# Optimization experiments

Hardware: AMD Instinct MI355X
Metric: run time of the kernel (lower is better)

Reference implementation:

```python
import jax, jax.numpy as jnp
import numpy as np

ROUTING_ITERS = 3


def squash(s):
    # s: [..., O]; magnitude squashed into (0, 1)
    sq_norm = jnp.sum(s * s, axis=-1, keepdims=True)
    return (sq_norm / (1.0 + sq_norm)) * s / jnp.sqrt(sq_norm)


def setup_inputs() -> dict:
    key = jax.random.key(0)
    k1, k2 = jax.random.split(key)
    B, P, CI, N, CO = 512, 1152, 8, 10, 16
    x = jax.random.normal(k1, (B, P, CI), dtype=jnp.float32)
    W = jax.random.normal(k2, (N, P, CI, CO), dtype=jnp.float32)
    return {"x": x, "W": W}


def reference(x, W):
    # x: [B, P, CI], W: [N, P, CI, CO]
    # torch: u_hat = (x[None,:,:,None,:] @ W[:,None]) -> [N, B, P, 1, CO];
    # we drop the singleton dim: u_hat [N, B, P, CO]
    u_hat = jnp.einsum('bpi,npio->nbpo', x, W)
    b_ij = jnp.zeros_like(u_hat)
    v_j = None
    for it in range(ROUTING_ITERS):
        # softmax over previous-layer nodes P (torch dim=2 of [N,B,P,1,CO])
        c_ij = jax.nn.softmax(b_ij, axis=2)
        s_j = jnp.sum(c_ij * u_hat, axis=2, keepdims=True)  # [N, B, 1, CO]
        v_j = squash(s_j)
        if it < ROUTING_ITERS - 1:
            a_ij = jnp.sum(u_hat * v_j, axis=-1, keepdims=True)  # [N, B, P, 1]
            b_ij = b_ij + a_ij
    return v_j  # [N, B, 1, CO]
```

## Files before the change

kernel.cpp:

```cpp
#include <hip/hip_runtime.h>
#include <cstddef>

#define NN 10
#define NB 512
#define NP 1152
#define CI 8
#define CO 16
#define BLOCK 256
#define BT 2
#define PT 18

__device__ __forceinline__ float wred_sum_pg(float v) {
#pragma unroll
  for (int m = 4; m <= 32; m <<= 1) v += __shfl_xor(v, m);
  return v;
}
__device__ __forceinline__ float wred_max_pg(float v) {
#pragma unroll
  for (int m = 4; m <= 32; m <<= 1) v = fmaxf(v, __shfl_xor(v, m));
  return v;
}

__global__ __launch_bounds__(BLOCK, 2)
void caps_kernel(const float* __restrict__ x, const float* __restrict__ W,
                 float* __restrict__ out) {
  const int tid  = threadIdx.x;
  const int lane = tid & 63;
  const int wid  = tid >> 6;
  const int o4   = (tid & 3) << 2;
  const int pg   = tid >> 2;

  const int bid = blockIdx.x;
  const int n   = bid >> 8;
  const int b0  = (bid & 255) * BT;

  __shared__ float sred[BT][4][CO];
  __shared__ float mred[BT][4];
  __shared__ float zred[BT][4];
  __shared__ float vbuf[BT][CO];

  float4 u[BT][PT];
  float  bl[BT][PT];

  const float* Wn  = W + (size_t)n * NP * CI * CO + o4;
  const float* xb0 = x + (size_t)b0 * NP * CI;

#pragma unroll
  for (int k = 0; k < PT; ++k) {
    const int p = pg + 64 * k;
    const float* wrow = Wn + p * (CI * CO);
    const float* xr   = xb0 + p * CI;
    float xv0[CI], xv1[CI];
    *(float4*)&xv0[0] = *(const float4*)(xr);
    *(float4*)&xv0[4] = *(const float4*)(xr + 4);
    *(float4*)&xv1[0] = *(const float4*)(xr + NP * CI);
    *(float4*)&xv1[4] = *(const float4*)(xr + NP * CI + 4);
    float4 a0 = make_float4(0.f, 0.f, 0.f, 0.f);
    float4 a1 = make_float4(0.f, 0.f, 0.f, 0.f);
#pragma unroll
    for (int i = 0; i < CI; ++i) {
      const float4 wv = *(const float4*)(wrow + i * CO);
      a0.x = fmaf(xv0[i], wv.x, a0.x);
      a0.y = fmaf(xv0[i], wv.y, a0.y);
      a0.z = fmaf(xv0[i], wv.z, a0.z);
      a0.w = fmaf(xv0[i], wv.w, a0.w);
      a1.x = fmaf(xv1[i], wv.x, a1.x);
      a1.y = fmaf(xv1[i], wv.y, a1.y);
      a1.z = fmaf(xv1[i], wv.z, a1.z);
      a1.w = fmaf(xv1[i], wv.w, a1.w);
    }
    u[0][k] = a0; u[1][k] = a1;
    bl[0][k] = 0.f; bl[1][k] = 0.f;
  }

  float4 vv[BT];
  float  mm[BT], rz[BT];

#pragma unroll 1
  for (int it = 0; it < 3; ++it) {
    if (it > 0) {
#pragma unroll
      for (int bt = 0; bt < BT; ++bt) {
#pragma unroll
        for (int k = 0; k < PT; ++k) {
          float d = u[bt][k].x * vv[bt].x + u[bt][k].y * vv[bt].y
                  + u[bt][k].z * vv[bt].z + u[bt][k].w * vv[bt].w;
          d += __shfl_xor(d, 1);
          d += __shfl_xor(d, 2);
          bl[bt][k] += d;
        }
      }
#pragma unroll
      for (int bt = 0; bt < BT; ++bt) {
        float m = bl[bt][0];
#pragma unroll
        for (int k = 1; k < PT; ++k) m = fmaxf(m, bl[bt][k]);
        m = wred_max_pg(m);
        if (lane == 0) mred[bt][wid] = m;
      }
      __syncthreads();
#pragma unroll
      for (int bt = 0; bt < BT; ++bt)
        mm[bt] = fmaxf(fmaxf(mred[bt][0], mred[bt][1]),
                       fmaxf(mred[bt][2], mred[bt][3]));
#pragma unroll
      for (int bt = 0; bt < BT; ++bt) {
        float z = 0.f;
#pragma unroll
        for (int k = 0; k < PT; ++k) z += __expf(bl[bt][k] - mm[bt]);
        z = wred_sum_pg(z);
        if (lane == 0) zred[bt][wid] = z;
      }
      __syncthreads();
#pragma unroll
      for (int bt = 0; bt < BT; ++bt) {
        const float SZ = zred[bt][0] + zred[bt][1] + zred[bt][2] + zred[bt][3];
        rz[bt] = 1.f / SZ;
      }
    }

#pragma unroll
    for (int bt = 0; bt < BT; ++bt) {
      float4 ps = make_float4(0.f, 0.f, 0.f, 0.f);
      if (it == 0) {
#pragma unroll
        for (int k = 0; k < PT; ++k) {
          ps.x += u[bt][k].x; ps.y += u[bt][k].y;
          ps.z += u[bt][k].z; ps.w += u[bt][k].w;
        }
        const float c = 1.f / (float)NP;
        ps.x *= c; ps.y *= c; ps.z *= c; ps.w *= c;
      } else {
#pragma unroll
        for (int k = 0; k < PT; ++k) {
          const float e = __expf(bl[bt][k] - mm[bt]);
          ps.x = fmaf(e, u[bt][k].x, ps.x);
          ps.y = fmaf(e, u[bt][k].y, ps.y);
          ps.z = fmaf(e, u[bt][k].z, ps.z);
          ps.w = fmaf(e, u[bt][k].w, ps.w);
        }
        ps.x *= rz[bt]; ps.y *= rz[bt]; ps.z *= rz[bt]; ps.w *= rz[bt];
      }
#pragma unroll
      for (int m = 4; m <= 32; m <<= 1) {
        ps.x += __shfl_xor(ps.x, m);
        ps.y += __shfl_xor(ps.y, m);
        ps.z += __shfl_xor(ps.z, m);
        ps.w += __shfl_xor(ps.w, m);
      }
      if (lane < 4) *(float4*)&sred[bt][wid][lane << 2] = ps;
    }
    __syncthreads();

    if (tid < 32) {
      const int bt = tid >> 4, o = tid & 15;
      float s = sred[bt][0][o] + sred[bt][1][o] + sred[bt][2][o] + sred[bt][3][o];
      float sq = s * s;
#pragma unroll
      for (int m = 1; m <= 8; m <<= 1) sq += __shfl_xor(sq, m);
      const float nrm = sqrtf(sq);
      const float vj  = s * (nrm / (1.f + sq));
      if (it == 2) out[((size_t)n * NB + b0 + bt) * CO + o] = vj;
      else         vbuf[bt][o] = vj;
    }
    if (it < 2) {
      __syncthreads();
#pragma unroll
      for (int bt = 0; bt < BT; ++bt) vv[bt] = *(const float4*)&vbuf[bt][o4];
    }
  }
}

extern "C" void kernel_launch(void* const* d_in, const int* in_sizes, int n_in,
                              void* d_out, int out_size, void* d_ws, size_t ws_size,
                              hipStream_t stream) {
  const float* x = (const float*)d_in[0];
  const float* W = (const float*)d_in[1];
  float* out     = (float*)d_out;
  (void)in_sizes; (void)n_in; (void)out_size; (void)d_ws; (void)ws_size;
  const int grid = NN * (NB / BT);
  caps_kernel<<<grid, BLOCK, 0, stream>>>(x, W, out);
}
```

Before: 329.5 us.

## Stage x tile in LDS and loop over output capsules per block

Each block now loads x for 4 batch rows into swizzled shared memory once and loops over 5 output capsules, reusing that x tile for every capsule and reusing each W load across 4 batch rows. Block size doubles to 512 threads, and the softmax max/sum and weighted-sum reductions are fused so there is one fewer barrier per iteration. The aim is to cut redundant global traffic on x and W. The cost is about 147KB of dynamic LDS per block, which limits occupancy, and a grid of only 256 blocks with serial per-capsule work.

```diff
diff --git a/kernel.cpp b/kernel.cpp
--- a/kernel.cpp
+++ b/kernel.cpp
@@ -6,168 +6,175 @@
 #define NP 1152
 #define CI 8
 #define CO 16
-#define BLOCK 256
-#define BT 2
-#define PT 18
+#define BLOCK 512
+#define BT 4
+#define NPER 5
+#define PSLOTS 128
+#define PT 9
+#define NWAVE 8
 
-__device__ __forceinline__ float wred_sum_pg(float v) {
-#pragma unroll
-  for (int m = 4; m <= 32; m <<= 1) v += __shfl_xor(v, m);
-  return v;
-}
-__device__ __forceinline__ float wred_max_pg(float v) {
-#pragma unroll
-  for (int m = 4; m <= 32; m <<= 1) v = fmaxf(v, __shfl_xor(v, m));
-  return v;
-}
+#define X_FLOATS (BT * NP * CI)
+#define SRED_OFF (X_FLOATS)
+#define ZRED_OFF (SRED_OFF + NWAVE * BT * CO)
+#define MZ_OFF   (ZRED_OFF + NWAVE * BT)
+#define VBUF_OFF (MZ_OFF + NWAVE * BT)
+#define SMEM_FLOATS (VBUF_OFF + BT * CO)
+#define SMEM_BYTES (SMEM_FLOATS * 4)
 
-__global__ __launch_bounds__(BLOCK, 2)
+__global__
+__attribute__((amdgpu_flat_work_group_size(BLOCK, BLOCK), amdgpu_waves_per_eu(2, 2)))
 void caps_kernel(const float* __restrict__ x, const float* __restrict__ W,
                  float* __restrict__ out) {
+  extern __shared__ float smem[];
+  float4* X4 = (float4*)smem;
+
   const int tid  = threadIdx.x;
   const int lane = tid & 63;
   const int wid  = tid >> 6;
   const int o4   = (tid & 3) << 2;
-  const int pg   = tid >> 2;
+  const int ps   = tid >> 2;
 
   const int bid = blockIdx.x;
-  const int n   = bid >> 8;
-  const int b0  = (bid & 255) * BT;
+  const int nh  = bid & 1;
+  const int b0  = (bid >> 1) * BT;
 
-  __shared__ float sred[BT][4][CO];
-  __shared__ float mred[BT][4];
-  __shared__ float zred[BT][4];
-  __shared__ float vbuf[BT][CO];
+  {
+    const float4* xg = (const float4*)(x + (size_t)b0 * NP * CI);
+#pragma unroll
+    for (int k = 0; k < 18; ++k) {
+      const int j = tid + BLOCK * k;
+      X4[j ^ ((j >> 3) & 1)] = xg[j];
+    }
+  }
+  __syncthreads();
 
-  float4 u[BT][PT];
-  float  bl[BT][PT];
+  for (int ni = 0; ni < NPER; ++ni) {
+    const int n = nh * NPER + ni;
+    const float* Wn = W + ((size_t)n * NP + ps) * (CI * CO) + o4;
 
-  const float* Wn  = W + (size_t)n * NP * CI * CO + o4;
-  const float* xb0 = x + (size_t)b0 * NP * CI;
+    float4 u[BT][PT];
+    float  bl[BT][PT];
 
 #pragma unroll
-  for (int k = 0; k < PT; ++k) {
-    const int p = pg + 64 * k;
-    const float* wrow = Wn + p * (CI * CO);
-    const float* xr   = xb0 + p * CI;
-    float xv0[CI], xv1[CI];
-    *(float4*)&xv0[0] = *(const float4*)(xr);
-    *(float4*)&xv0[4] = *(const float4*)(xr + 4);
-    *(float4*)&xv1[0] = *(const float4*)(xr + NP * CI);
-    *(float4*)&xv1[4] = *(const float4*)(xr + NP * CI + 4);
-    float4 a0 = make_float4(0.f, 0.f, 0.f, 0.f);
-    float4 a1 = make_float4(0.f, 0.f, 0.f, 0.f);
+    for (int k = 0; k < PT; ++k) {
+      const int p = ps + PSLOTS * k;
+      const float* wrow = Wn + (size_t)k * (PSLOTS * CI * CO);
+      float4 wv[CI];
 #pragma unroll
-    for (int i = 0; i < CI; ++i) {
-      const float4 wv = *(const float4*)(wrow + i * CO);
-      a0.x = fmaf(xv0[i], wv.x, a0.x);
-      a0.y = fmaf(xv0[i], wv.y, a0.y);
-      a0.z = fmaf(xv0[i], wv.z, a0.z);
-      a0.w = fmaf(xv0[i], wv.w, a0.w);
-      a1.x = fmaf(xv1[i], wv.x, a1.x);
-      a1.y = fmaf(xv1[i], wv.y, a1.y);
-      a1.z = fmaf(xv1[i], wv.z, a1.z);
-      a1.w = fmaf(xv1[i], wv.w, a1.w);
-    }
-    u[0][k] = a0; u[1][k] = a1;
-    bl[0][k] = 0.f; bl[1][k] = 0.f;
-  }
-
-  float4 vv[BT];
-  float  mm[BT], rz[BT];
-
-#pragma unroll 1
-  for (int it = 0; it < 3; ++it) {
-    if (it > 0) {
+      for (int i = 0; i < CI; ++i) wv[i] = *(const float4*)(wrow + i * CO);
+      const int sw = (p >> 2) & 1;
 #pragma unroll
-      for (int bt = 0; bt < BT; ++bt) {
+      for (int b = 0; b < BT; ++b) {
+        const int c0 = (b * NP + p) << 1;
+        float xi[CI];
+        *(float4*)&xi[0] = X4[c0 ^ sw];
+        *(float4*)&xi[4] = X4[(c0 | 1) ^ sw];
+        float4 a = make_float4(0.f, 0.f, 0.f, 0.f);
 #pragma unroll
-        for (int k = 0; k < PT; ++k) {
-          float d = u[bt][k].x * vv[bt].x + u[bt][k].y * vv[bt].y
-                  + u[bt][k].z * vv[bt].z + u[bt][k].w * vv[bt].w;
-          d += __shfl_xor(d, 1);
-          d += __shfl_xor(d, 2);
-          bl[bt][k] += d;
+        for (int i = 0; i < CI; ++i) {
+          a.x = fmaf(xi[i], wv[i].x, a.x);
+          a.y = fmaf(xi[i], wv[i].y, a.y);
+          a.z = fmaf(xi[i], wv[i].z, a.z);
+          a.w = fmaf(xi[i], wv[i].w, a.w);
         }
-      }
-#pragma unroll
-      for (int bt = 0; bt < BT; ++bt) {
-        float m = bl[bt][0];
-#pragma unroll
-        for (int k = 1; k < PT; ++k) m = fmaxf(m, bl[bt][k]);
-        m = wred_max_pg(m);
-        if (lane == 0) mred[bt][wid] = m;
-      }
-      __syncthreads();
-#pragma unroll
-      for (int bt = 0; bt < BT; ++bt)
-        mm[bt] = fmaxf(fmaxf(mred[bt][0], mred[bt][1]),
-                       fmaxf(mred[bt][2], mred[bt][3]));
-#pragma unroll
-      for (int bt = 0; bt < BT; ++bt) {
-        float z = 0.f;
-#pragma unroll
-        for (int k = 0; k < PT; ++k) z += __expf(bl[bt][k] - mm[bt]);
-        z = wred_sum_pg(z);
-        if (lane == 0) zred[bt][wid] = z;
-      }
-      __syncthreads();
-#pragma unroll
-      for (int bt = 0; bt < BT; ++bt) {
-        const float SZ = zred[bt][0] + zred[bt][1] + zred[bt][2] + zred[bt][3];
-        rz[bt] = 1.f / SZ;
+        u[b][k] = a;
+        bl[b][k] = 0.f;
       }
     }
 
+    float4 vvb[BT];
+    float  mm[BT];
+
+#pragma unroll 1
+    for (int it = 0; it < 3; ++it) {
+      if (it > 0) {
 #pragma unroll
-    for (int bt = 0; bt < BT; ++bt) {
-      float4 ps = make_float4(0.f, 0.f, 0.f, 0.f);
-      if (it == 0) {
+        for (int b = 0; b < BT; ++b) {
+          float m = -1e30f;
 #pragma unroll
-        for (int k = 0; k < PT; ++k) {
-          ps.x += u[bt][k].x; ps.y += u[bt][k].y;
-          ps.z += u[bt][k].z; ps.w += u[bt][k].w;
+          for (int k = 0; k < PT; ++k) {
+            float d = u[b][k].x * vvb[b].x + u[b][k].y * vvb[b].y
+                    + u[b][k].z * vvb[b].z + u[b][k].w * vvb[b].w;
+            d += __shfl_xor(d, 1);
+            d += __shfl_xor(d, 2);
+            const float nb2 = bl[b][k] + d;
+            bl[b][k] = nb2;
+            m = fmaxf(m, nb2);
+          }
+#pragma unroll
+          for (int s = 4; s <= 32; s <<= 1) m = fmaxf(m, __shfl_xor(m, s));
+          if (lane == 0) smem[MZ_OFF + wid * BT + b] = m;
         }
-        const float c = 1.f / (float)NP;
-        ps.x *= c; ps.y *= c; ps.z *= c; ps.w *= c;
-      } else {
+        __syncthreads();
 #pragma unroll
-        for (int k = 0; k < PT; ++k) {
-          const float e = __expf(bl[bt][k] - mm[bt]);
-          ps.x = fmaf(e, u[bt][k].x, ps.x);
-          ps.y = fmaf(e, u[bt][k].y, ps.y);
-          ps.z = fmaf(e, u[bt][k].z, ps.z);
-          ps.w = fmaf(e, u[bt][k].w, ps.w);
+        for (int b = 0; b < BT; ++b) {
+          float m = smem[MZ_OFF + b];
+#pragma unroll
+          for (int w = 1; w < NWAVE; ++w) m = fmaxf(m, smem[MZ_OFF + w * BT + b]);
+          mm[b] = m;
         }
-        ps.x *= rz[bt]; ps.y *= rz[bt]; ps.z *= rz[bt]; ps.w *= rz[bt];
       }
+
 #pragma unroll
-      for (int m = 4; m <= 32; m <<= 1) {
-        ps.x += __shfl_xor(ps.x, m);
-        ps.y += __shfl_xor(ps.y, m);
-        ps.z += __shfl_xor(ps.z, m);
-        ps.w += __shfl_xor(ps.w, m);
+      for (int b = 0; b < BT; ++b) {
+        float z = 0.f;
+        float4 ps4 = make_float4(0.f, 0.f, 0.f, 0.f);
+        if (it == 0) {
+#pragma unroll
+          for (int k = 0; k < PT; ++k) {
+            z += 1.f;
+            ps4.x += u[b][k].x; ps4.y += u[b][k].y;
+            ps4.z += u[b][k].z; ps4.w += u[b][k].w;
+          }
+        } else {
+#pragma unroll
+          for (int k = 0; k < PT; ++k) {
+            const float e = __expf(bl[b][k] - mm[b]);
+            z += e;
+            ps4.x = fmaf(e, u[b][k].x, ps4.x);
+            ps4.y = fmaf(e, u[b][k].y, ps4.y);
+            ps4.z = fmaf(e, u[b][k].z, ps4.z);
+            ps4.w = fmaf(e, u[b][k].w, ps4.w);
+          }
+        }
+#pragma unroll
+        for (int s = 4; s <= 32; s <<= 1) {
+          ps4.x += __shfl_xor(ps4.x, s);
+          ps4.y += __shfl_xor(ps4.y, s);
+          ps4.z += __shfl_xor(ps4.z, s);
+          ps4.w += __shfl_xor(ps4.w, s);
+          z     += __shfl_xor(z, s);
+        }
+        if (lane < 4)  *(float4*)&smem[SRED_OFF + (wid * BT + b) * CO + (lane << 2)] = ps4;
+        if (lane == 0) smem[ZRED_OFF + wid * BT + b] = z;
       }
-      if (lane < 4) *(float4*)&sred[bt][wid][lane << 2] = ps;
+      __syncthreads();
+
+      if (tid < 64) {
+        const int b = tid >> 4, o = tid & 15;
+        float s = 0.f, Z = 0.f;
+#pragma unroll
+        for (int w = 0; w < NWAVE; ++w) {
+          s += smem[SRED_OFF + (w * BT + b) * CO + o];
+          Z += smem[ZRED_OFF + w * BT + b];
+        }
+        s /= Z;
+        float sq = s * s;
+#pragma unroll
+        for (int m2 = 1; m2 <= 8; m2 <<= 1) sq += __shfl_xor(sq, m2);
+        const float nrm = sqrtf(sq);
+        const float vj  = s * (nrm / (1.f + sq));
+        if (it == 2) out[((size_t)n * NB + b0 + b) * CO + o] = vj;
+        else         smem[VBUF_OFF + b * CO + o] = vj;
+      }
+      if (it < 2) {
+        __syncthreads();
+#pragma unroll
+        for (int b = 0; b < BT; ++b)
+          vvb[b] = *(const float4*)&smem[VBUF_OFF + b * CO + o4];
+      }
     }
     __syncthreads();
-
-    if (tid < 32) {
-      const int bt = tid >> 4, o = tid & 15;
-      float s = sred[bt][0][o] + sred[bt][1][o] + sred[bt][2][o] + sred[bt][3][o];
-      float sq = s * s;
-#pragma unroll
-      for (int m = 1; m <= 8; m <<= 1) sq += __shfl_xor(sq, m);
-      const float nrm = sqrtf(sq);
-      const float vj  = s * (nrm / (1.f + sq));
-      if (it == 2) out[((size_t)n * NB + b0 + bt) * CO + o] = vj;
-      else         vbuf[bt][o] = vj;
-    }
-    if (it < 2) {
-      __syncthreads();
-#pragma unroll
-      for (int bt = 0; bt < BT; ++bt) vv[bt] = *(const float4*)&vbuf[bt][o4];
-    }
   }
 }
 
@@ -178,6 +185,10 @@
   const float* W = (const float*)d_in[1];
   float* out     = (float*)d_out;
   (void)in_sizes; (void)n_in; (void)out_size; (void)d_ws; (void)ws_size;
-  const int grid = NN * (NB / BT);
-  caps_kernel<<<grid, BLOCK, 0, stream>>>(x, W, out);
+
+  hipFuncSetAttribute((const void*)caps_kernel,
+                      hipFuncAttributeMaxDynamicSharedMemorySize, SMEM_BYTES);
+
+  const int grid = (NB / BT) * 2;
+  caps_kernel<<<grid, BLOCK, SMEM_BYTES, stream>>>(x, W, out);
 }
```

After: 464.1 us. 40.8% more time.
